# Performance work log

Hardware: AMD Instinct MI355X
Metric: run time of the kernel (lower is better)

Reference implementation:

```python
import jax, jax.numpy as jnp
import numpy as np

N_NODES = 50000
N_EDGES = 1600000
NODE_DIM = 1024
HID = 128
OUT = 128
LN_EPS = 1e-5


def setup_inputs() -> dict:
    key = jax.random.key(0)
    ks = jax.random.split(key, 8)
    s = lambda d: 1.0 / np.sqrt(d)
    return {
        "x": jax.random.normal(ks[0], (N_NODES, NODE_DIM), jnp.float32),
        "edge_index": jax.random.randint(ks[1], (2, N_EDGES), 0, N_NODES, jnp.int64),
        "proj_w": jax.random.normal(ks[2], (HID, NODE_DIM), jnp.float32) * s(NODE_DIM),
        "proj_b": jnp.zeros((HID,), jnp.float32),
        "lin_l_w": jax.random.normal(ks[3], (HID, HID), jnp.float32) * s(HID),
        "lin_l_b": jnp.zeros((HID,), jnp.float32),
        "lin_r_w": jax.random.normal(ks[4], (HID, HID), jnp.float32) * s(HID),
        "ln_g": jnp.ones((HID,), jnp.float32),
        "ln_b": jnp.zeros((HID,), jnp.float32),
        "out_w": jax.random.normal(ks[5], (OUT, HID), jnp.float32) * s(HID),
        "out_b": jnp.zeros((OUT,), jnp.float32),
    }


def reference(x, edge_index, proj_w, proj_b, lin_l_w, lin_l_b, lin_r_w, ln_g, ln_b, out_w, out_b):
    n = x.shape[0]
    # input projection + ReLU: [N, node_dim] -> [N, H]
    h = jax.nn.relu(x @ proj_w.T + proj_b)
    # SAGEConv(mean): gather source features, mean-scatter to targets
    src, dst = edge_index[0], edge_index[1]
    agg = jax.ops.segment_sum(h[src], dst, num_segments=n)  # [N, H]
    deg = jax.ops.segment_sum(jnp.ones((src.shape[0],), h.dtype), dst, num_segments=n)
    mean_nbr = agg / jnp.maximum(deg, 1.0)[:, None]
    h = mean_nbr @ lin_l_w.T + lin_l_b + h @ lin_r_w.T
    # LayerNorm over feature dim
    mu = h.mean(-1, keepdims=True)
    var = jnp.mean((h - mu) ** 2, -1, keepdims=True)
    h = (h - mu) * jax.lax.rsqrt(var + LN_EPS) * ln_g + ln_b
    h = jax.nn.relu(h)  # dropout is identity in eval
    # batch=None -> global mean pool over all nodes: [1, H]
    g = h.mean(0, keepdims=True)
    return g @ out_w.T + out_b
```

## Files before the change

### kernel.cpp

```cpp
#include <hip/hip_runtime.h>

#define N_NODES  50000
#define N_EDGES  1600000
#define NODE_DIM 1024
#define HID      128
#define LN_EPS   1e-5f
#define NBUCK    196
#define SHARD    6250

typedef float f32x4 __attribute__((ext_vector_type(4)));
typedef __bf16 bf16x8 __attribute__((ext_vector_type(8)));
typedef unsigned short u16x8 __attribute__((ext_vector_type(8)));

__device__ __forceinline__ unsigned short f2bf(float f) {
  __bf16 b = (__bf16)f;
  return __builtin_bit_cast(unsigned short, b);
}
__device__ __forceinline__ unsigned int pkbf(float a, float b) {
  return (unsigned int)f2bf(a) | ((unsigned int)f2bf(b) << 16);
}
__device__ __forceinline__ float bf2f(unsigned short v) {
  return __uint_as_float((unsigned int)v << 16);
}

__device__ __forceinline__ int scan256_excl(int v, int buf[2][256], int t) {
  int cur = 0;
  buf[0][t] = v;
  __syncthreads();
  for (int off = 1; off < 256; off <<= 1) {
    int nxt = cur ^ 1;
    int s = buf[cur][t];
    if (t >= off) s += buf[cur][t - off];
    buf[nxt][t] = s;
    cur = nxt;
    __syncthreads();
  }
  return buf[cur][t] - v;
}

__global__ __launch_bounds__(256) void k_proj(const float* __restrict__ x,
                                              const float* __restrict__ pw,
                                              const float* __restrict__ pb,
                                              unsigned short* __restrict__ h) {
  __shared__ unsigned short As[2][128][32];
  __shared__ unsigned short Bs[2][128][32];
  const int tid = threadIdx.x;
  const int m0 = blockIdx.x * 128;
  const int wave = tid >> 6, lane = tid & 63;
  const int wm = (wave >> 1) * 64, wn = (wave & 1) * 64;
  const int srow = tid >> 1;
  const int sub  = tid & 1;
  const int fr = lane & 15, ko = (lane >> 4) * 8;

  f32x4 acc[4][4] = {};
  const int arow = m0 + srow;
  const bool aval = (arow < N_NODES);
  const float* xrow = x + (size_t)arow * NODE_DIM + sub * 32;
  const float* brow = pw + (size_t)srow * NODE_DIM + sub * 32;

  for (int k0 = 0; k0 < NODE_DIM; k0 += 64) {
    float4 av[8], bv[8];
    if (aval) {
      const float4* p = (const float4*)(xrow + k0);
#pragma unroll
      for (int j = 0; j < 8; j++) av[j] = p[j];
    } else {
#pragma unroll
      for (int j = 0; j < 8; j++) av[j] = make_float4(0.f, 0.f, 0.f, 0.f);
    }
    const float4* q = (const float4*)(brow + k0);
#pragma unroll
    for (int j = 0; j < 8; j++) bv[j] = q[j];

    __syncthreads();
    unsigned int* da = (unsigned int*)&As[sub][srow][0];
    unsigned int* db = (unsigned int*)&Bs[sub][srow][0];
#pragma unroll
    for (int j = 0; j < 8; j++) {
      da[2 * j]     = pkbf(av[j].x, av[j].y);
      da[2 * j + 1] = pkbf(av[j].z, av[j].w);
      db[2 * j]     = pkbf(bv[j].x, bv[j].y);
      db[2 * j + 1] = pkbf(bv[j].z, bv[j].w);
    }
    __syncthreads();

#pragma unroll
    for (int s = 0; s < 2; s++) {
      bf16x8 af[4], bfr[4];
#pragma unroll
      for (int m = 0; m < 4; m++)
        af[m] = *(const bf16x8*)&As[s][wm + m * 16 + fr][ko];
#pragma unroll
      for (int n = 0; n < 4; n++)
        bfr[n] = *(const bf16x8*)&Bs[s][wn + n * 16 + fr][ko];
#pragma unroll
      for (int m = 0; m < 4; m++)
#pragma unroll
        for (int n = 0; n < 4; n++)
          acc[m][n] = __builtin_amdgcn_mfma_f32_16x16x32_bf16(af[m], bfr[n], acc[m][n], 0, 0, 0);
    }
  }

  const int cr = (lane >> 4) * 4, cc = lane & 15;
#pragma unroll
  for (int n = 0; n < 4; n++) {
    const int col = wn + n * 16 + cc;
    const float bias = pb[col];
#pragma unroll
    for (int m = 0; m < 4; m++) {
#pragma unroll
      for (int i = 0; i < 4; i++) {
        const int row = m0 + wm + m * 16 + cr + i;
        if (row < N_NODES) {
          float v = acc[m][n][i] + bias;
          h[(size_t)row * HID + col] = f2bf(v > 0.f ? v : 0.f);
        }
      }
    }
  }
}

__global__ __launch_bounds__(256) void k_hist(const int* __restrict__ ei,
                                              int* __restrict__ counts) {
  __shared__ int bins[NBUCK];
  int t = threadIdx.x;
  if (t < NBUCK) bins[t] = 0;
  __syncthreads();
  int base = blockIdx.x * SHARD;
  for (int i = t; i < SHARD; i += 256)
    atomicAdd(&bins[ei[N_EDGES + base + i] >> 8], 1);
  __syncthreads();
  if (t < NBUCK) counts[t * 256 + blockIdx.x] = bins[t];
}

__global__ __launch_bounds__(256) void k_s1(const int* __restrict__ counts,
                                            int* __restrict__ basem,
                                            int* __restrict__ btot) {
  __shared__ int buf[2][256];
  int t = threadIdx.x, b = blockIdx.x;
  int v = counts[b * 256 + t];
  int excl = scan256_excl(v, buf, t);
  basem[b * 256 + t] = excl;
  if (t == 255) btot[b] = excl + v;
}

__global__ __launch_bounds__(256) void k_s2(const int* __restrict__ btot,
                                            int* __restrict__ bstart,
                                            float* __restrict__ accum) {
  __shared__ int buf[2][256];
  int t = threadIdx.x;
  int v = (t < NBUCK) ? btot[t] : 0;
  int excl = scan256_excl(v, buf, t);
  if (t < NBUCK) bstart[t] = excl;
  if (t == 0) bstart[NBUCK] = N_EDGES;
  if (t < HID) accum[t] = 0.f;
}

__global__ __launch_bounds__(256) void k_scatter(const int* __restrict__ ei,
                                                 const int* __restrict__ basem,
                                                 const int* __restrict__ bstart,
                                                 unsigned int* __restrict__ bs) {
  __shared__ int cur[NBUCK];
  int t = threadIdx.x;
  if (t < NBUCK) cur[t] = bstart[t] + basem[t * 256 + blockIdx.x];
  __syncthreads();
  int base = blockIdx.x * SHARD;
  for (int i = t; i < SHARD; i += 256) {
    int e = base + i;
    unsigned int src = (unsigned int)ei[e];
    unsigned int dst = (unsigned int)ei[N_EDGES + e];
    int pos = atomicAdd(&cur[dst >> 8], 1);
    bs[pos] = src | ((dst & 255u) << 16);
  }
}

__global__ __launch_bounds__(256) void k_bucket(const int* __restrict__ bstart,
                                                const unsigned int* __restrict__ bs,
                                                unsigned short* __restrict__ nbr,
                                                int* __restrict__ offs,
                                                int* __restrict__ deg) {
  __shared__ int bins[256];
  __shared__ int buf[2][256];
  __shared__ int curs[256];
  int t = threadIdx.x, b = blockIdx.x;
  int s = bstart[b], e = bstart[b + 1];
  bins[t] = 0;
  __syncthreads();
  for (int i = s + t; i < e; i += 256)
    atomicAdd(&bins[(bs[i] >> 16) & 255u], 1);
  __syncthreads();
  int v = bins[t];
  int excl = scan256_excl(v, buf, t);
  int node = b * 256 + t;
  deg[node]  = v;
  offs[node] = s + excl;
  curs[t]    = s + excl;
  __syncthreads();
  for (int i = s + t; i < e; i += 256) {
    unsigned int p = bs[i];
    int pos = atomicAdd(&curs[(p >> 16) & 255u], 1);
    nbr[pos] = (unsigned short)(p & 0xffffu);
  }
}

__global__ __launch_bounds__(256) void k_gather(const unsigned short* __restrict__ h,
                                                const unsigned short* __restrict__ nbr,
                                                const int* __restrict__ offs,
                                                const int* __restrict__ deg,
                                                unsigned short* __restrict__ mn) {
  const int wave = threadIdx.x >> 6;
  const int lane = threadIdx.x & 63;
  const int node = blockIdx.x * 4 + wave;
  if (node >= N_NODES) return;
  const int g = lane >> 4, li = lane & 15;
  const int d  = deg[node];
  const int st = offs[node];
  float a[8] = {0.f, 0.f, 0.f, 0.f, 0.f, 0.f, 0.f, 0.f};
  int n = g;
  for (; n + 4 < d; n += 8) {
    int s0 = nbr[st + n];
    int s1 = nbr[st + n + 4];
    u16x8 v0 = *(const u16x8*)(h + (size_t)s0 * HID + li * 8);
    u16x8 v1 = *(const u16x8*)(h + (size_t)s1 * HID + li * 8);
#pragma unroll
    for (int k = 0; k < 8; k++) a[k] += bf2f(v0[k]) + bf2f(v1[k]);
  }
  if (n < d) {
    int s0 = nbr[st + n];
    u16x8 v0 = *(const u16x8*)(h + (size_t)s0 * HID + li * 8);
#pragma unroll
    for (int k = 0; k < 8; k++) a[k] += bf2f(v0[k]);
  }
#pragma unroll
  for (int k = 0; k < 8; k++) {
    a[k] += __shfl_xor(a[k], 16);
    a[k] += __shfl_xor(a[k], 32);
  }
  if (g == 0) {
    float inv = 1.f / fmaxf((float)d, 1.f);
    u16x8 r;
#pragma unroll
    for (int k = 0; k < 8; k++) r[k] = f2bf(a[k] * inv);
    *(u16x8*)(mn + (size_t)node * HID + li * 8) = r;
  }
}

__global__ __launch_bounds__(256) void k_sage(const unsigned short* __restrict__ mn,
                                              const unsigned short* __restrict__ h,
                                              const float* __restrict__ wl,
                                              const float* __restrict__ wr,
                                              const float* __restrict__ lb,
                                              const float* __restrict__ lg,
                                              const float* __restrict__ lbt,
                                              float* __restrict__ accum) {
  __shared__ unsigned short As[128 * 32];
  __shared__ unsigned short Bs[128 * 32];
  __shared__ float T3[32 * 128];
  __shared__ float red[4][128];
  const int tid = threadIdx.x;
  const int m0 = blockIdx.x * 128;
  const int wave = tid >> 6, lane = tid & 63;
  const int wm = (wave >> 1) * 64, wn = (wave & 1) * 64;
  const int srow = tid >> 1, scol = (tid & 1) * 16;
  const int fr = lane & 15, ko = (lane >> 4) * 8;

  f32x4 acc[4][4] = {};

  for (int k0 = 0; k0 < 2 * HID; k0 += 32) {
    const unsigned short* baseA = (k0 < HID) ? mn : h;
    const float* baseB = (k0 < HID) ? wl : wr;
    const int kk = (k0 & (HID - 1)) + scol;
    const int arow = m0 + srow;
    u16x8 a0 = {0, 0, 0, 0, 0, 0, 0, 0}, a1 = a0;
    if (arow < N_NODES) {
      const u16x8* p = (const u16x8*)(baseA + (size_t)arow * HID + kk);
      a0 = p[0]; a1 = p[1];
    }
    const float4* q = (const float4*)(baseB + (size_t)srow * HID + kk);
    float4 b0 = q[0], b1 = q[1], b2 = q[2], b3 = q[3];

    __syncthreads();
    *(u16x8*)&As[srow * 32 + scol]     = a0;
    *(u16x8*)&As[srow * 32 + scol + 8] = a1;
    unsigned int* db = (unsigned int*)&Bs[srow * 32 + scol];
    db[0] = pkbf(b0.x, b0.y); db[1] = pkbf(b0.z, b0.w);
    db[2] = pkbf(b1.x, b1.y); db[3] = pkbf(b1.z, b1.w);
    db[4] = pkbf(b2.x, b2.y); db[5] = pkbf(b2.z, b2.w);
    db[6] = pkbf(b3.x, b3.y); db[7] = pkbf(b3.z, b3.w);
    __syncthreads();

    bf16x8 af[4], bfr[4];
#pragma unroll
    for (int m = 0; m < 4; m++)
      af[m] = *(const bf16x8*)&As[(wm + m * 16 + fr) * 32 + ko];
#pragma unroll
    for (int n = 0; n < 4; n++)
      bfr[n] = *(const bf16x8*)&Bs[(wn + n * 16 + fr) * 32 + ko];
#pragma unroll
    for (int m = 0; m < 4; m++)
#pragma unroll
      for (int n = 0; n < 4; n++)
        acc[m][n] = __builtin_amdgcn_mfma_f32_16x16x32_bf16(af[m], bfr[n], acc[m][n], 0, 0, 0);
  }

  const int cr = (lane >> 4) * 4, cc = lane & 15;
  const int p = wave >> 1;
  const float g0 = lg[lane], g1 = lg[lane + 64];
  const float t0 = lbt[lane], t1 = lbt[lane + 64];
  float ax = 0.f, ay = 0.f;
#pragma unroll
  for (int m = 0; m < 4; m++) {
    __syncthreads();
#pragma unroll
    for (int n = 0; n < 4; n++) {
      const int col = wn + n * 16 + cc;
      const float bias = lb[col];
#pragma unroll
      for (int i = 0; i < 4; i++)
        T3[(p * 16 + cr + i) * 128 + col] = acc[m][n][i] + bias;
    }
    __syncthreads();
    for (int r8 = 0; r8 < 8; r8++) {
      int q8 = wave * 8 + r8;
      int grow = m0 + (q8 >> 4) * 64 + m * 16 + (q8 & 15);
      float v0 = T3[q8 * 128 + lane];
      float v1 = T3[q8 * 128 + lane + 64];
      float sum = v0 + v1, ss = v0 * v0 + v1 * v1;
#pragma unroll
      for (int off = 32; off > 0; off >>= 1) {
        sum += __shfl_xor(sum, off);
        ss  += __shfl_xor(ss, off);
      }
      float mu  = sum * (1.f / HID);
      float var = ss * (1.f / HID) - mu * mu;
      float rinv = rsqrtf(var + LN_EPS);
      if (grow < N_NODES) {
        float y0 = (v0 - mu) * rinv * g0 + t0;
        float y1 = (v1 - mu) * rinv * g1 + t1;
        ax += fmaxf(y0, 0.f);
        ay += fmaxf(y1, 0.f);
      }
    }
  }
  red[wave][lane]      = ax;
  red[wave][lane + 64] = ay;
  __syncthreads();
  if (wave == 0) {
    float a  = red[0][lane] + red[1][lane] + red[2][lane] + red[3][lane];
    float bb = red[0][lane + 64] + red[1][lane + 64] + red[2][lane + 64] + red[3][lane + 64];
    atomicAdd(&accum[lane], a);
    atomicAdd(&accum[lane + 64], bb);
  }
}

__global__ __launch_bounds__(128) void k_final(const float* __restrict__ accum,
                                               const float* __restrict__ ow,
                                               const float* __restrict__ ob,
                                               float* __restrict__ out) {
  __shared__ float gs[HID];
  int t = threadIdx.x;
  gs[t] = accum[t] * (1.f / N_NODES);
  __syncthreads();
  float s = ob[t];
  for (int k = 0; k < HID; k++) s += gs[k] * ow[t * HID + k];
  out[t] = s;
}

extern "C" void kernel_launch(void* const* d_in, const int* in_sizes, int n_in,
                              void* d_out, int out_size, void* d_ws, size_t ws_size,
                              hipStream_t stream) {
  const float* x   = (const float*)d_in[0];
  const int*   ei  = (const int*)d_in[1];
  const float* pw  = (const float*)d_in[2];
  const float* pb  = (const float*)d_in[3];
  const float* wl  = (const float*)d_in[4];
  const float* lb  = (const float*)d_in[5];
  const float* wr  = (const float*)d_in[6];
  const float* lg  = (const float*)d_in[7];
  const float* lbt = (const float*)d_in[8];
  const float* ow  = (const float*)d_in[9];
  const float* ob  = (const float*)d_in[10];
  float* out = (float*)d_out;

  const int PAD = NBUCK * 256;
  unsigned short* h  = (unsigned short*)d_ws;
  unsigned short* mn = h + (size_t)PAD * HID;
  unsigned int* bsp  = (unsigned int*)(mn + (size_t)PAD * HID);
  unsigned short* nbr = (unsigned short*)(bsp + N_EDGES);
  int* counts = (int*)(nbr + N_EDGES);
  int* basem  = counts + NBUCK * 256;
  int* btot   = basem + NBUCK * 256;
  int* bstart = btot + 256;
  int* offs   = bstart + 256;
  int* deg    = offs + PAD;
  float* accum = (float*)(deg + PAD);

  const int MB = (N_NODES + 127) / 128;

  hipLaunchKernelGGL(k_proj,    dim3(MB),    dim3(256), 0, stream, x, pw, pb, h);
  hipLaunchKernelGGL(k_hist,    dim3(256),   dim3(256), 0, stream, ei, counts);
  hipLaunchKernelGGL(k_s1,      dim3(NBUCK), dim3(256), 0, stream, counts, basem, btot);
  hipLaunchKernelGGL(k_s2,      dim3(1),     dim3(256), 0, stream, btot, bstart, accum);
  hipLaunchKernelGGL(k_scatter, dim3(256),   dim3(256), 0, stream, ei, basem, bstart, bsp);
  hipLaunchKernelGGL(k_bucket,  dim3(NBUCK), dim3(256), 0, stream, bstart, bsp, nbr, offs, deg);
  hipLaunchKernelGGL(k_gather,  dim3((N_NODES + 3) / 4), dim3(256), 0, stream, h, nbr, offs, deg, mn);
  hipLaunchKernelGGL(k_sage,    dim3(MB),    dim3(256), 0, stream, mn, h, wl, wr, lb, lg, lbt, accum);
  hipLaunchKernelGGL(k_final,   dim3(1),     dim3(128), 0, stream, accum, ow, ob, out);
}
```

Before: 473.8 us.

## Pre-convert projection weights to bf16, halve M tile, prefetch next K slab

Adds a small kernel that converts the projection weight matrix to bf16 once per call, so k_proj loads bf16 weights directly instead of converting them from fp32 in every block. The projection tile shrinks from 128 to 64 rows, doubling the grid to about 782 blocks for better CU occupancy. Shared memory rows are padded to 40 elements to reduce bank conflicts. Global loads for the next K slab are issued before the MFMA work on the current one so memory latency overlaps compute. The trade-offs are more total weight traffic across the larger grid, one extra launch, and a smaller per-wave MFMA tile.

After: 475.6 us. About the same (+0.4%).

```diff
diff --git a/kernel.cpp b/kernel.cpp
--- a/kernel.cpp
+++ b/kernel.cpp
@@ -38,63 +38,81 @@
   return buf[cur][t] - v;
 }
 
+__global__ __launch_bounds__(256) void k_wcvt(const float* __restrict__ w,
+                                              unsigned short* __restrict__ wb) {
+  int i = (blockIdx.x * 256 + threadIdx.x) * 4;
+  float4 v = *(const float4*)(w + i);
+  unsigned int* o = (unsigned int*)(wb + i);
+  o[0] = pkbf(v.x, v.y);
+  o[1] = pkbf(v.z, v.w);
+}
+
+#define LDR 40
+
 __global__ __launch_bounds__(256) void k_proj(const float* __restrict__ x,
-                                              const float* __restrict__ pw,
+                                              const unsigned short* __restrict__ pwb,
                                               const float* __restrict__ pb,
                                               unsigned short* __restrict__ h) {
-  __shared__ unsigned short As[2][128][32];
-  __shared__ unsigned short Bs[2][128][32];
+  __shared__ unsigned short As[2 * 64 * LDR];
+  __shared__ unsigned short Bs[2 * 128 * LDR];
   const int tid = threadIdx.x;
-  const int m0 = blockIdx.x * 128;
+  const int m0 = blockIdx.x * 64;
   const int wave = tid >> 6, lane = tid & 63;
-  const int wm = (wave >> 1) * 64, wn = (wave & 1) * 64;
-  const int srow = tid >> 1;
-  const int sub  = tid & 1;
+  const int wm = (wave >> 1) * 32, wn = (wave & 1) * 64;
   const int fr = lane & 15, ko = (lane >> 4) * 8;
 
-  f32x4 acc[4][4] = {};
-  const int arow = m0 + srow;
-  const bool aval = (arow < N_NODES);
-  const float* xrow = x + (size_t)arow * NODE_DIM + sub * 32;
-  const float* brow = pw + (size_t)srow * NODE_DIM + sub * 32;
-
+  const int arow = tid >> 2, akq = (tid & 3) * 16;
+  const int grow = m0 + arow;
+  const bool aval = (grow < N_NODES);
+  const float* aptr = x + (size_t)grow * NODE_DIM + akq;
+  const int brow = tid >> 1, bkq = (tid & 1) * 32;
+  const unsigned short* bptr = pwb + (size_t)brow * NODE_DIM + bkq;
+
+  f32x4 acc[2][4] = {};
+  float4 av[4];
+  u16x8 bv[4];
+
+  auto LOAD = [&](int k0) {
+    if (aval) {
+      const float4* p = (const float4*)(aptr + k0);
+#pragma unroll
+      for (int j = 0; j < 4; j++) av[j] = p[j];
+    } else {
+#pragma unroll
+      for (int j = 0; j < 4; j++) av[j] = make_float4(0.f, 0.f, 0.f, 0.f);
+    }
+    const u16x8* q = (const u16x8*)(bptr + k0);
+#pragma unroll
+    for (int j = 0; j < 4; j++) bv[j] = q[j];
+  };
+
+  LOAD(0);
   for (int k0 = 0; k0 < NODE_DIM; k0 += 64) {
-    float4 av[8], bv[8];
-    if (aval) {
-      const float4* p = (const float4*)(xrow + k0);
-#pragma unroll
-      for (int j = 0; j < 8; j++) av[j] = p[j];
-    } else {
-#pragma unroll
-      for (int j = 0; j < 8; j++) av[j] = make_float4(0.f, 0.f, 0.f, 0.f);
-    }
-    const float4* q = (const float4*)(brow + k0);
-#pragma unroll
-    for (int j = 0; j < 8; j++) bv[j] = q[j];
-
-    __syncthreads();
-    unsigned int* da = (unsigned int*)&As[sub][srow][0];
-    unsigned int* db = (unsigned int*)&Bs[sub][srow][0];
-#pragma unroll
-    for (int j = 0; j < 8; j++) {
+    __syncthreads();
+    unsigned int* da = (unsigned int*)&As[((akq >> 5) * 64 + arow) * LDR + (akq & 31)];
+#pragma unroll
+    for (int j = 0; j < 4; j++) {
       da[2 * j]     = pkbf(av[j].x, av[j].y);
       da[2 * j + 1] = pkbf(av[j].z, av[j].w);
-      db[2 * j]     = pkbf(bv[j].x, bv[j].y);
-      db[2 * j + 1] = pkbf(bv[j].z, bv[j].w);
-    }
-    __syncthreads();
+    }
+    u16x8* db = (u16x8*)&Bs[((bkq >> 5) * 128 + brow) * LDR];
+#pragma unroll
+    for (int j = 0; j < 4; j++) db[j] = bv[j];
+    __syncthreads();
+
+    if (k0 + 64 < NODE_DIM) LOAD(k0 + 64);
 
 #pragma unroll
     for (int s = 0; s < 2; s++) {
-      bf16x8 af[4], bfr[4];
-#pragma unroll
-      for (int m = 0; m < 4; m++)
-        af[m] = *(const bf16x8*)&As[s][wm + m * 16 + fr][ko];
+      bf16x8 af[2], bfr[4];
+#pragma unroll
+      for (int m = 0; m < 2; m++)
+        af[m] = *(const bf16x8*)&As[(s * 64 + wm + m * 16 + fr) * LDR + ko];
 #pragma unroll
       for (int n = 0; n < 4; n++)
-        bfr[n] = *(const bf16x8*)&Bs[s][wn + n * 16 + fr][ko];
-#pragma unroll
-      for (int m = 0; m < 4; m++)
+        bfr[n] = *(const bf16x8*)&Bs[(s * 128 + wn + n * 16 + fr) * LDR + ko];
+#pragma unroll
+      for (int m = 0; m < 2; m++)
 #pragma unroll
         for (int n = 0; n < 4; n++)
           acc[m][n] = __builtin_amdgcn_mfma_f32_16x16x32_bf16(af[m], bfr[n], acc[m][n], 0, 0, 0);
@@ -107,7 +125,7 @@
     const int col = wn + n * 16 + cc;
     const float bias = pb[col];
 #pragma unroll
-    for (int m = 0; m < 4; m++) {
+    for (int m = 0; m < 2; m++) {
 #pragma unroll
       for (int i = 0; i < 4; i++) {
         const int row = m0 + wm + m * 16 + cr + i;
@@ -394,10 +412,13 @@
   int* offs   = bstart + 256;
   int* deg    = offs + PAD;
   float* accum = (float*)(deg + PAD);
-
-  const int MB = (N_NODES + 127) / 128;
-
-  hipLaunchKernelGGL(k_proj,    dim3(MB),    dim3(256), 0, stream, x, pw, pb, h);
+  unsigned short* pwb = (unsigned short*)(accum + 128);
+
+  const int MB  = (N_NODES + 127) / 128;
+  const int MB2 = (N_NODES + 63) / 64;
+
+  hipLaunchKernelGGL(k_wcvt,    dim3(HID * NODE_DIM / 1024), dim3(256), 0, stream, pw, pwb);
+  hipLaunchKernelGGL(k_proj,    dim3(MB2),   dim3(256), 0, stream, x, pwb, pb, h);
   hipLaunchKernelGGL(k_hist,    dim3(256),   dim3(256), 0, stream, ei, counts);
   hipLaunchKernelGGL(k_s1,      dim3(NBUCK), dim3(256), 0, stream, counts, basem, btot);
   hipLaunchKernelGGL(k_s2,      dim3(1),     dim3(256), 0, stream, btot, bstart, accum);
```

## Prepack projection weights into MFMA fragment layout and stream x directly to registers

Applied to the files above, without the earlier changes.

A new kernel converts the projection weights to bf16 once, in the per-lane fragment order the MFMA instructions expect. The projection kernel drops its LDS staging and block-wide barriers: each wave owns a 32-row strip, loads x straight into registers with double-buffered prefetch, and reads the prepacked weights as vector loads. The output is 32x128 per wave, launched as 392 blocks with a launch-bounds occupancy hint, and the projection now runs after the bucketing kernels. Weight tiles are no longer shared across waves through LDS, so weight traffic goes to L2 instead, and the last strip writes rows up to 50175, which relies on the padded h buffer.

New measurement: 473.6 us. Within noise of the previous version (-0.0%).

```diff
diff --git a/kernel.cpp b/kernel.cpp
--- a/kernel.cpp
+++ b/kernel.cpp
@@ -11,6 +11,7 @@
 typedef float f32x4 __attribute__((ext_vector_type(4)));
 typedef __bf16 bf16x8 __attribute__((ext_vector_type(8)));
 typedef unsigned short u16x8 __attribute__((ext_vector_type(8)));
+typedef unsigned int u32x4 __attribute__((ext_vector_type(4)));
 
 __device__ __forceinline__ unsigned short f2bf(float f) {
   __bf16 b = (__bf16)f;
@@ -38,83 +39,90 @@
   return buf[cur][t] - v;
 }
 
-__global__ __launch_bounds__(256) void k_proj(const float* __restrict__ x,
-                                              const float* __restrict__ pw,
-                                              const float* __restrict__ pb,
-                                              unsigned short* __restrict__ h) {
-  __shared__ unsigned short As[2][128][32];
-  __shared__ unsigned short Bs[2][128][32];
-  const int tid = threadIdx.x;
-  const int m0 = blockIdx.x * 128;
-  const int wave = tid >> 6, lane = tid & 63;
-  const int wm = (wave >> 1) * 64, wn = (wave & 1) * 64;
-  const int srow = tid >> 1;
-  const int sub  = tid & 1;
-  const int fr = lane & 15, ko = (lane >> 4) * 8;
-
-  f32x4 acc[4][4] = {};
-  const int arow = m0 + srow;
-  const bool aval = (arow < N_NODES);
-  const float* xrow = x + (size_t)arow * NODE_DIM + sub * 32;
-  const float* brow = pw + (size_t)srow * NODE_DIM + sub * 32;
-
-  for (int k0 = 0; k0 < NODE_DIM; k0 += 64) {
-    float4 av[8], bv[8];
-    if (aval) {
-      const float4* p = (const float4*)(xrow + k0);
-#pragma unroll
-      for (int j = 0; j < 8; j++) av[j] = p[j];
-    } else {
-#pragma unroll
-      for (int j = 0; j < 8; j++) av[j] = make_float4(0.f, 0.f, 0.f, 0.f);
-    }
-    const float4* q = (const float4*)(brow + k0);
-#pragma unroll
-    for (int j = 0; j < 8; j++) bv[j] = q[j];
-
-    __syncthreads();
-    unsigned int* da = (unsigned int*)&As[sub][srow][0];
-    unsigned int* db = (unsigned int*)&Bs[sub][srow][0];
-#pragma unroll
-    for (int j = 0; j < 8; j++) {
-      da[2 * j]     = pkbf(av[j].x, av[j].y);
-      da[2 * j + 1] = pkbf(av[j].z, av[j].w);
-      db[2 * j]     = pkbf(bv[j].x, bv[j].y);
-      db[2 * j + 1] = pkbf(bv[j].z, bv[j].w);
-    }
-    __syncthreads();
-
-#pragma unroll
-    for (int s = 0; s < 2; s++) {
-      bf16x8 af[4], bfr[4];
-#pragma unroll
-      for (int m = 0; m < 4; m++)
-        af[m] = *(const bf16x8*)&As[s][wm + m * 16 + fr][ko];
-#pragma unroll
-      for (int n = 0; n < 4; n++)
-        bfr[n] = *(const bf16x8*)&Bs[s][wn + n * 16 + fr][ko];
-#pragma unroll
-      for (int m = 0; m < 4; m++)
-#pragma unroll
-        for (int n = 0; n < 4; n++)
-          acc[m][n] = __builtin_amdgcn_mfma_f32_16x16x32_bf16(af[m], bfr[n], acc[m][n], 0, 0, 0);
-    }
-  }
+__global__ __launch_bounds__(256) void k_wpack(const float* __restrict__ w,
+                                               unsigned short* __restrict__ wp) {
+  int idx = blockIdx.x * 256 + threadIdx.x;
+  int lane = idx & 63;
+  int n = (idx >> 6) & 7;
+  int ks = idx >> 9;
+  int fr = lane & 15, kg = lane >> 4;
+  const float* src = w + (size_t)(n * 16 + fr) * NODE_DIM + ks * 32 + kg * 8;
+  float4 v0 = *(const float4*)(src);
+  float4 v1 = *(const float4*)(src + 4);
+  unsigned int* o = (unsigned int*)(wp + (size_t)idx * 8);
+  o[0] = pkbf(v0.x, v0.y);
+  o[1] = pkbf(v0.z, v0.w);
+  o[2] = pkbf(v1.x, v1.y);
+  o[3] = pkbf(v1.z, v1.w);
+}
+
+__global__ __launch_bounds__(256, 3) void k_proj(const float* __restrict__ x,
+                                                 const unsigned short* __restrict__ wp,
+                                                 const float* __restrict__ pb,
+                                                 unsigned short* __restrict__ h) {
+  const int wave = threadIdx.x >> 6, lane = threadIdx.x & 63;
+  const int fr = lane & 15, kg = lane >> 4;
+  const int strip = blockIdx.x * 4 + wave;
+  const int m0 = strip * 32;
+
+  int r0 = m0 + fr;      if (r0 >= N_NODES) r0 = N_NODES - 1;
+  int r1 = m0 + 16 + fr; if (r1 >= N_NODES) r1 = N_NODES - 1;
+  const float* a0p = x + (size_t)r0 * NODE_DIM + kg * 8;
+  const float* a1p = x + (size_t)r1 * NODE_DIM + kg * 8;
+  const bf16x8* bp = (const bf16x8*)wp + lane;
+
+  f32x4 acc[2][8] = {};
+
+  float4 xa0, xa1, xa2, xa3;
+  float4 ya0, ya1, ya2, ya3;
+
+#define LOADA_X(KS) { const float* p0 = a0p + (KS) * 32; const float* p1 = a1p + (KS) * 32; \
+  xa0 = *(const float4*)p0; xa1 = *(const float4*)(p0 + 4); \
+  xa2 = *(const float4*)p1; xa3 = *(const float4*)(p1 + 4); }
+#define LOADA_Y(KS) { const float* p0 = a0p + (KS) * 32; const float* p1 = a1p + (KS) * 32; \
+  ya0 = *(const float4*)p0; ya1 = *(const float4*)(p0 + 4); \
+  ya2 = *(const float4*)p1; ya3 = *(const float4*)(p1 + 4); }
+
+#define COMPUTE(A0, A1, A2, A3, KS) { \
+  bf16x8 bfv[8]; \
+  _Pragma("unroll") \
+  for (int n = 0; n < 8; n++) bfv[n] = bp[((KS) * 8 + n) * 64]; \
+  u32x4 pa0, pa1; \
+  pa0[0] = pkbf(A0.x, A0.y); pa0[1] = pkbf(A0.z, A0.w); \
+  pa0[2] = pkbf(A1.x, A1.y); pa0[3] = pkbf(A1.z, A1.w); \
+  pa1[0] = pkbf(A2.x, A2.y); pa1[1] = pkbf(A2.z, A2.w); \
+  pa1[2] = pkbf(A3.x, A3.y); pa1[3] = pkbf(A3.z, A3.w); \
+  bf16x8 af0 = __builtin_bit_cast(bf16x8, pa0); \
+  bf16x8 af1 = __builtin_bit_cast(bf16x8, pa1); \
+  _Pragma("unroll") \
+  for (int n = 0; n < 8; n++) { \
+    acc[0][n] = __builtin_amdgcn_mfma_f32_16x16x32_bf16(af0, bfv[n], acc[0][n], 0, 0, 0); \
+    acc[1][n] = __builtin_amdgcn_mfma_f32_16x16x32_bf16(af1, bfv[n], acc[1][n], 0, 0, 0); \
+  } }
+
+  LOADA_X(0);
+  for (int ks = 0; ks < 32; ks += 2) {
+    LOADA_Y(ks + 1);
+    COMPUTE(xa0, xa1, xa2, xa3, ks);
+    if (ks + 2 < 32) LOADA_X(ks + 2);
+    COMPUTE(ya0, ya1, ya2, ya3, ks + 1);
+  }
+#undef LOADA_X
+#undef LOADA_Y
+#undef COMPUTE
 
   const int cr = (lane >> 4) * 4, cc = lane & 15;
 #pragma unroll
-  for (int n = 0; n < 4; n++) {
-    const int col = wn + n * 16 + cc;
+  for (int n = 0; n < 8; n++) {
+    const int col = n * 16 + cc;
     const float bias = pb[col];
 #pragma unroll
-    for (int m = 0; m < 4; m++) {
+    for (int m = 0; m < 2; m++) {
+      const int rowb = m0 + m * 16 + cr;
 #pragma unroll
       for (int i = 0; i < 4; i++) {
-        const int row = m0 + wm + m * 16 + cr + i;
-        if (row < N_NODES) {
-          float v = acc[m][n][i] + bias;
-          h[(size_t)row * HID + col] = f2bf(v > 0.f ? v : 0.f);
-        }
+        float v = acc[m][n][i] + bias;
+        h[(size_t)(rowb + i) * HID + col] = f2bf(v > 0.f ? v : 0.f);
       }
     }
   }
@@ -394,15 +402,19 @@
   int* offs   = bstart + 256;
   int* deg    = offs + PAD;
   float* accum = (float*)(deg + PAD);
-
-  const int MB = (N_NODES + 127) / 128;
-
-  hipLaunchKernelGGL(k_proj,    dim3(MB),    dim3(256), 0, stream, x, pw, pb, h);
+  unsigned short* wp = (unsigned short*)(accum + 128);
+
+  const int MB  = (N_NODES + 127) / 128;
+  const int PB  = (N_NODES + 127) / 128;
+  (void)PB;
+
+  hipLaunchKernelGGL(k_wpack,   dim3(64),    dim3(256), 0, stream, pw, wp);
   hipLaunchKernelGGL(k_hist,    dim3(256),   dim3(256), 0, stream, ei, counts);
   hipLaunchKernelGGL(k_s1,      dim3(NBUCK), dim3(256), 0, stream, counts, basem, btot);
   hipLaunchKernelGGL(k_s2,      dim3(1),     dim3(256), 0, stream, btot, bstart, accum);
   hipLaunchKernelGGL(k_scatter, dim3(256),   dim3(256), 0, stream, ei, basem, bstart, bsp);
   hipLaunchKernelGGL(k_bucket,  dim3(NBUCK), dim3(256), 0, stream, bstart, bsp, nbr, offs, deg);
+  hipLaunchKernelGGL(k_proj,    dim3(392),   dim3(256), 0, stream, x, wp, pb, h);
   hipLaunchKernelGGL(k_gather,  dim3((N_NODES + 3) / 4), dim3(256), 0, stream, h, nbr, offs, deg, mn);
   hipLaunchKernelGGL(k_sage,    dim3(MB),    dim3(256), 0, stream, mn, h, wl, wr, lb, lg, lbt, accum);
   hipLaunchKernelGGL(k_final,   dim3(1),     dim3(128), 0, stream, accum, ow, ob, out);
```
